# Kernel tuning notes

Hardware: AMD Instinct MI355X
Metric: run time of the kernel (lower is better)

## Reference

```python
import jax, jax.numpy as jnp
import numpy as np

B, T, F, H, E = 32, 512, 64, 64, 32  # batch, time, features(=sequence_length), hidden_dim, encoding_size


def setup_inputs() -> dict:
    key = jax.random.key(0)
    ks = jax.random.split(key, 14)
    sc = 0.05
    return {
        "x": jax.random.normal(ks[0], (B, T, F), jnp.float32),
        "s": jax.random.normal(ks[1], (B, T, E), jnp.float32),
        # gating FFN params
        "ffn_w1": jax.random.normal(ks[2], (F, H), jnp.float32) * sc,
        "ffn_b1": jnp.zeros((H,), jnp.float32),
        "ffn_w2": jax.random.normal(ks[3], (E, H), jnp.float32) * sc,
        "ffn_b2": jnp.zeros((H,), jnp.float32),
        "ffn_w3": jax.random.normal(ks[4], (H, F), jnp.float32) * sc,
        "ffn_b3": jnp.zeros((F,), jnp.float32),
        # per-feature expert FFN_j params (F experts, each Dense(1->H), ELU, Dense(H->H))
        "exp_w1": jax.random.normal(ks[5], (F, H), jnp.float32) * sc,  # weight of Dense(1->H) per feature
        "exp_b1": jnp.zeros((F, H), jnp.float32),
        "exp_w3": jax.random.normal(ks[6], (F, H, H), jnp.float32) * sc,
        "exp_b3": jnp.zeros((F, H), jnp.float32),
    }


def reference(x, s, ffn_w1, ffn_b1, ffn_w2, ffn_b2, ffn_w3, ffn_b3,
              exp_w1, exp_b1, exp_w3, exp_b3):
    # gating network: softmax over feature axis
    g = jnp.einsum('btf,fh->bth', x, ffn_w1) + ffn_b1 \
        + jnp.einsum('bte,eh->bth', s, ffn_w2) + ffn_b2
    logits = jnp.einsum('bth,hf->btf', jax.nn.elu(g), ffn_w3) + ffn_b3
    w_t = jax.nn.softmax(logits, axis=2)  # [B,T,F]

    # per-feature experts, batched: Dense(1->H) is a rank-1 outer product
    h = jax.nn.elu(x[..., None] * exp_w1[None, None] + exp_b1[None, None])  # [B,T,F,H]
    expert_out = jnp.einsum('btfh,fhk->btfk', h, exp_w3) + exp_b3[None, None]  # [B,T,F,H]

    # gate-weighted sum over features
    return jnp.einsum('btfk,btf->btk', expert_out, w_t)  # [B,T,H]
```

## Files before the change

### kernel.cpp

```cpp
#include <hip/hip_runtime.h>
#include <hip/hip_bf16.h>
#include <math.h>

#define NTOK 16384

typedef __attribute__((ext_vector_type(8))) short short8;
typedef __attribute__((ext_vector_type(4))) float f32x4;

__device__ __forceinline__ unsigned pack_bf16(float a, float b) {
    union { __hip_bfloat162 h; unsigned u; } cv;
    cv.h = __float22bfloat162_rn(make_float2(a, b));
    return cv.u;
}
__device__ __forceinline__ float eluf(float z) {
    return z > 0.0f ? z : (__expf(z) - 1.0f);
}

__global__ __launch_bounds__(256)
void prepass(const float* __restrict__ ew3, const float* __restrict__ eb3,
             unsigned short* __restrict__ ws) {
    __shared__ float tile[64 * 65];
    const int bid = blockIdx.x, tid = threadIdx.x;
    const float* src = (bid < 64) ? (ew3 + (size_t)bid * 4096) : eb3;

    const int r = tid >> 2, c0 = (tid & 3) * 16;
    #pragma unroll
    for (int j = 0; j < 4; ++j) {
        float4 v = *(const float4*)(src + r * 64 + c0 + j * 4);
        tile[r * 65 + c0 + j * 4 + 0] = v.x;
        tile[r * 65 + c0 + j * 4 + 1] = v.y;
        tile[r * 65 + c0 + j * 4 + 2] = v.z;
        tile[r * 65 + c0 + j * 4 + 3] = v.w;
    }
    __syncthreads();

    uint4* dst = (uint4*)(ws + (size_t)bid * 4096);
    #pragma unroll
    for (int it = 0; it < 2; ++it) {
        const int idx = tid + it * 256;
        const int c = idx >> 8, u = (idx >> 6) & 3, l = idx & 63;
        const int m = l & 15, q = (l >> 4) & 3;
        const int rb = c * 32 + q * 8, col = u * 16 + m;
        unsigned pw[4];
        #pragma unroll
        for (int p = 0; p < 4; ++p)
            pw[p] = pack_bf16(tile[(rb + 2 * p) * 65 + col],
                              tile[(rb + 2 * p + 1) * 65 + col]);
        uint4 pk; pk.x = pw[0]; pk.y = pw[1]; pk.z = pw[2]; pk.w = pw[3];
        dst[idx] = pk;
    }
}

__device__ __forceinline__ void gen_a2(const float* __restrict__ ew1,
                                       const float* __restrict__ eb1,
                                       int f, int quad,
                                       float xv0, float wt0, float xv1, float wt1,
                                       short8* a0, short8* a1) {
    #pragma unroll
    for (int c = 0; c < 2; ++c) {
        const float* w1p = ew1 + f * 64 + c * 32 + quad * 8;
        const float* b1p = eb1 + f * 64 + c * 32 + quad * 8;
        const float4 wa = *(const float4*)w1p, wb = *(const float4*)(w1p + 4);
        const float4 ba = *(const float4*)b1p, bb = *(const float4*)(b1p + 4);
        uint4 v0, v1;
        v0.x = pack_bf16(wt0 * eluf(fmaf(xv0, wa.x, ba.x)),
                         wt0 * eluf(fmaf(xv0, wa.y, ba.y)));
        v0.y = pack_bf16(wt0 * eluf(fmaf(xv0, wa.z, ba.z)),
                         wt0 * eluf(fmaf(xv0, wa.w, ba.w)));
        v0.z = pack_bf16(wt0 * eluf(fmaf(xv0, wb.x, bb.x)),
                         wt0 * eluf(fmaf(xv0, wb.y, bb.y)));
        v0.w = pack_bf16(wt0 * eluf(fmaf(xv0, wb.z, bb.z)),
                         wt0 * eluf(fmaf(xv0, wb.w, bb.w)));
        v1.x = pack_bf16(wt1 * eluf(fmaf(xv1, wa.x, ba.x)),
                         wt1 * eluf(fmaf(xv1, wa.y, ba.y)));
        v1.y = pack_bf16(wt1 * eluf(fmaf(xv1, wa.z, ba.z)),
                         wt1 * eluf(fmaf(xv1, wa.w, ba.w)));
        v1.z = pack_bf16(wt1 * eluf(fmaf(xv1, wb.x, bb.x)),
                         wt1 * eluf(fmaf(xv1, wb.y, bb.y)));
        v1.w = pack_bf16(wt1 * eluf(fmaf(xv1, wb.z, bb.z)),
                         wt1 * eluf(fmaf(xv1, wb.w, bb.w)));
        a0[c] = *(short8*)&v0;
        a1[c] = *(short8*)&v1;
    }
}

__global__ __launch_bounds__(512, 6)
void moe_main(const float* __restrict__ x,   const float* __restrict__ s,
              const float* __restrict__ fw1, const float* __restrict__ fb1,
              const float* __restrict__ fw2, const float* __restrict__ fb2,
              const float* __restrict__ fw3, const float* __restrict__ fb3,
              const float* __restrict__ ew1, const float* __restrict__ eb1,
              const float* __restrict__ ew3, const float* __restrict__ eb3,
              const unsigned short* __restrict__ img,
              float* __restrict__ out)
{
    __shared__ __align__(16) char smem[51840];
    float* xls = (float*)smem;
    float* wts = (float*)(smem + 8704);
    float* egs = (float*)(smem + 17024);
    float* ped0 = (float*)(smem + 17024);
    float* ped1 = (float*)(smem + 17024 + 17408);

    const int tid = threadIdx.x;
    const int wv = tid >> 6, lane = tid & 63;
    const int m = tid & 15, quad = (tid >> 4) & 3;
    const int tokbase = blockIdx.x * 32;

    {
        const int t = tid >> 4, fq = (tid & 15) * 4;
        *(float4*)&xls[t * 68 + fq] =
            *(const float4*)(x + (size_t)(tokbase + t) * 64 + fq);
    }
    __syncthreads();

    {
        const int t0w = wv * 4;
        const float* sw = s + (size_t)(tokbase + t0w) * 32;
        float g[4];
        const float b0 = fb1[lane] + fb2[lane];
        #pragma unroll
        for (int t = 0; t < 4; ++t) g[t] = b0;
        #pragma unroll 2
        for (int f = 0; f < 64; f += 4) {
            const float w0 = fw1[(f + 0) * 64 + lane];
            const float w1 = fw1[(f + 1) * 64 + lane];
            const float w2 = fw1[(f + 2) * 64 + lane];
            const float w3v = fw1[(f + 3) * 64 + lane];
            #pragma unroll
            for (int t = 0; t < 4; ++t) {
                const float4 xa = *(const float4*)&xls[(t0w + t) * 68 + f];
                g[t] = fmaf(xa.x, w0, fmaf(xa.y, w1, fmaf(xa.z, w2, fmaf(xa.w, w3v, g[t]))));
            }
        }
        #pragma unroll 2
        for (int e = 0; e < 32; e += 4) {
            const float w0 = fw2[(e + 0) * 64 + lane];
            const float w1 = fw2[(e + 1) * 64 + lane];
            const float w2 = fw2[(e + 2) * 64 + lane];
            const float w3v = fw2[(e + 3) * 64 + lane];
            #pragma unroll
            for (int t = 0; t < 4; ++t) {
                const float4 sa = *(const float4*)(sw + t * 32 + e);
                g[t] = fmaf(sa.x, w0, fmaf(sa.y, w1, fmaf(sa.z, w2, fmaf(sa.w, w3v, g[t]))));
            }
        }
        #pragma unroll
        for (int t = 0; t < 4; ++t) egs[(t0w + t) * 64 + lane] = eluf(g[t]);

        float lg[4];
        const float b3 = fb3[lane];
        #pragma unroll
        for (int t = 0; t < 4; ++t) lg[t] = b3;
        #pragma unroll 2
        for (int h = 0; h < 64; h += 4) {
            const float w0 = fw3[(h + 0) * 64 + lane];
            const float w1 = fw3[(h + 1) * 64 + lane];
            const float w2 = fw3[(h + 2) * 64 + lane];
            const float w3v = fw3[(h + 3) * 64 + lane];
            #pragma unroll
            for (int t = 0; t < 4; ++t) {
                const float4 ev = *(const float4*)&egs[(t0w + t) * 64 + h];
                lg[t] = fmaf(ev.x, w0, fmaf(ev.y, w1, fmaf(ev.z, w2, fmaf(ev.w, w3v, lg[t]))));
            }
        }
        #pragma unroll
        for (int t = 0; t < 4; ++t) {
            float mx = lg[t];
            #pragma unroll
            for (int off = 32; off > 0; off >>= 1) mx = fmaxf(mx, __shfl_xor(mx, off));
            const float p = __expf(lg[t] - mx);
            float sm = p;
            #pragma unroll
            for (int off = 32; off > 0; off >>= 1) sm += __shfl_xor(sm, off);
            wts[(t0w + t) * 65 + lane] = p / sm;
        }
    }
    __syncthreads();

    const int f0 = wv * 8;
    f32x4 acc0[4], acc1[4];
    #pragma unroll
    for (int u = 0; u < 4; ++u) {
        acc0[u] = (f32x4){0.f, 0.f, 0.f, 0.f};
        acc1[u] = (f32x4){0.f, 0.f, 0.f, 0.f};
    }

    const uint4* bp = (const uint4*)img + (size_t)f0 * 512 + lane;
    #pragma unroll 1
    for (int ff = 0; ff < 8; ++ff) {
        const int f = f0 + ff;
        uint4 b0 = bp[0 * 64];
        uint4 b1 = bp[1 * 64];
        uint4 b2 = bp[2 * 64];
        uint4 b3 = bp[3 * 64];
        uint4 b4 = bp[256 + 0 * 64];
        uint4 b5 = bp[256 + 1 * 64];
        uint4 b6 = bp[256 + 2 * 64];
        uint4 b7 = bp[256 + 3 * 64];
        bp += 512;
        const float xv0 = xls[m * 68 + f];
        const float wt0 = wts[m * 65 + f];
        const float xv1 = xls[(16 + m) * 68 + f];
        const float wt1 = wts[(16 + m) * 65 + f];
        short8 a0[2], a1[2];
        gen_a2(ew1, eb1, f, quad, xv0, wt0, xv1, wt1, a0, a1);
        acc0[0] = __builtin_amdgcn_mfma_f32_16x16x32_bf16(a0[0], *(short8*)&b0, acc0[0], 0, 0, 0);
        acc0[1] = __builtin_amdgcn_mfma_f32_16x16x32_bf16(a0[0], *(short8*)&b1, acc0[1], 0, 0, 0);
        acc0[2] = __builtin_amdgcn_mfma_f32_16x16x32_bf16(a0[0], *(short8*)&b2, acc0[2], 0, 0, 0);
        acc0[3] = __builtin_amdgcn_mfma_f32_16x16x32_bf16(a0[0], *(short8*)&b3, acc0[3], 0, 0, 0);
        acc1[0] = __builtin_amdgcn_mfma_f32_16x16x32_bf16(a1[0], *(short8*)&b0, acc1[0], 0, 0, 0);
        acc1[1] = __builtin_amdgcn_mfma_f32_16x16x32_bf16(a1[0], *(short8*)&b1, acc1[1], 0, 0, 0);
        acc1[2] = __builtin_amdgcn_mfma_f32_16x16x32_bf16(a1[0], *(short8*)&b2, acc1[2], 0, 0, 0);
        acc1[3] = __builtin_amdgcn_mfma_f32_16x16x32_bf16(a1[0], *(short8*)&b3, acc1[3], 0, 0, 0);
        acc0[0] = __builtin_amdgcn_mfma_f32_16x16x32_bf16(a0[1], *(short8*)&b4, acc0[0], 0, 0, 0);
        acc0[1] = __builtin_amdgcn_mfma_f32_16x16x32_bf16(a0[1], *(short8*)&b5, acc0[1], 0, 0, 0);
        acc0[2] = __builtin_amdgcn_mfma_f32_16x16x32_bf16(a0[1], *(short8*)&b6, acc0[2], 0, 0, 0);
        acc0[3] = __builtin_amdgcn_mfma_f32_16x16x32_bf16(a0[1], *(short8*)&b7, acc0[3], 0, 0, 0);
        acc1[0] = __builtin_amdgcn_mfma_f32_16x16x32_bf16(a1[1], *(short8*)&b4, acc1[0], 0, 0, 0);
        acc1[1] = __builtin_amdgcn_mfma_f32_16x16x32_bf16(a1[1], *(short8*)&b5, acc1[1], 0, 0, 0);
        acc1[2] = __builtin_amdgcn_mfma_f32_16x16x32_bf16(a1[1], *(short8*)&b6, acc1[2], 0, 0, 0);
        acc1[3] = __builtin_amdgcn_mfma_f32_16x16x32_bf16(a1[1], *(short8*)&b7, acc1[3], 0, 0, 0);
    }

    if (wv < 4) {
        const int tile = wv >> 1, eh = wv & 1;
        const int e0 = eh * 32 + quad * 8;
        const int trow = tile * 16 + m;
        uint4 av;
        av.x = pack_bf16(wts[trow * 65 + e0 + 0], wts[trow * 65 + e0 + 1]);
        av.y = pack_bf16(wts[trow * 65 + e0 + 2], wts[trow * 65 + e0 + 3]);
        av.z = pack_bf16(wts[trow * 65 + e0 + 4], wts[trow * 65 + e0 + 5]);
        av.w = pack_bf16(wts[trow * 65 + e0 + 6], wts[trow * 65 + e0 + 7]);
        short8 a = *(short8*)&av;
        const uint4* bq = (const uint4*)img + (size_t)64 * 512;
        f32x4* accT = tile ? acc1 : acc0;
        #pragma unroll
        for (int u = 0; u < 4; ++u) {
            uint4 bv = bq[eh * 256 + u * 64 + lane];
            accT[u] = __builtin_amdgcn_mfma_f32_16x16x32_bf16(a, *(short8*)&bv, accT[u], 0, 0, 0);
        }
    }

    if (wv >= 4) {
        #pragma unroll
        for (int u = 0; u < 4; ++u)
            #pragma unroll
            for (int r = 0; r < 4; ++r) {
                const int idx = (quad * 4 + r) * 68 + u * 16 + m;
                ped0[(wv - 4) * 1088 + idx] = acc0[u][r];
                ped1[(wv - 4) * 1088 + idx] = acc1[u][r];
            }
    }
    __syncthreads();
    if (wv < 4) {
        #pragma unroll
        for (int u = 0; u < 4; ++u)
            #pragma unroll
            for (int r = 0; r < 4; ++r) {
                const int idx = (quad * 4 + r) * 68 + u * 16 + m;
                acc0[u][r] += ped0[wv * 1088 + idx];
                acc1[u][r] += ped1[wv * 1088 + idx];
            }
    }
    __syncthreads();
    if (wv == 2 || wv == 3) {
        #pragma unroll
        for (int u = 0; u < 4; ++u)
            #pragma unroll
            for (int r = 0; r < 4; ++r) {
                const int idx = (quad * 4 + r) * 68 + u * 16 + m;
                ped0[(wv - 2) * 1088 + idx] = acc0[u][r];
                ped1[(wv - 2) * 1088 + idx] = acc1[u][r];
            }
    }
    __syncthreads();
    if (wv < 2) {
        #pragma unroll
        for (int u = 0; u < 4; ++u)
            #pragma unroll
            for (int r = 0; r < 4; ++r) {
                const int idx = (quad * 4 + r) * 68 + u * 16 + m;
                acc0[u][r] += ped0[wv * 1088 + idx];
                acc1[u][r] += ped1[wv * 1088 + idx];
            }
    }
    __syncthreads();
    if (wv == 1) {
        #pragma unroll
        for (int u = 0; u < 4; ++u)
            #pragma unroll
            for (int r = 0; r < 4; ++r) {
                const int idx = (quad * 4 + r) * 68 + u * 16 + m;
                ped0[idx] = acc0[u][r];
                ped1[idx] = acc1[u][r];
            }
    }
    __syncthreads();
    if (wv == 0) {
        #pragma unroll
        for (int u = 0; u < 4; ++u)
            #pragma unroll
            for (int r = 0; r < 4; ++r) {
                const int idx = (quad * 4 + r) * 68 + u * 16 + m;
                ped0[idx] += acc0[u][r];
                ped1[idx] += acc1[u][r];
            }
    }
    __syncthreads();

    {
        const int t = tid >> 4, kq = tid & 15;
        const float* srcp = (t < 16) ? &ped0[t * 68 + kq * 4]
                                     : &ped1[(t - 16) * 68 + kq * 4];
        *(float4*)(out + (size_t)(tokbase + t) * 64 + kq * 4) = *(const float4*)srcp;
    }
}

__device__ __forceinline__ void gen_a_fb(const float* __restrict__ ew1,
                                         const float* __restrict__ eb1,
                                         int f, int quad, float xv, float wt,
                                         short8* a) {
    #pragma unroll
    for (int c = 0; c < 2; ++c) {
        const float* w1p = ew1 + f * 64 + c * 32 + quad * 8;
        const float* b1p = eb1 + f * 64 + c * 32 + quad * 8;
        const float4 w1a = *(const float4*)w1p, w1b = *(const float4*)(w1p + 4);
        const float4 b1a = *(const float4*)b1p, b1b = *(const float4*)(b1p + 4);
        uint4 av;
        av.x = pack_bf16(wt * eluf(fmaf(xv, w1a.x, b1a.x)),
                         wt * eluf(fmaf(xv, w1a.y, b1a.y)));
        av.y = pack_bf16(wt * eluf(fmaf(xv, w1a.z, b1a.z)),
                         wt * eluf(fmaf(xv, w1a.w, b1a.w)));
        av.z = pack_bf16(wt * eluf(fmaf(xv, w1b.x, b1b.x)),
                         wt * eluf(fmaf(xv, w1b.y, b1b.y)));
        av.w = pack_bf16(wt * eluf(fmaf(xv, w1b.z, b1b.z)),
                         wt * eluf(fmaf(xv, w1b.w, b1b.w)));
        a[c] = *(short8*)&av;
    }
}
__device__ __forceinline__ void gen_b_fp32(const float* __restrict__ w3f,
                                           int quad, int m, short8 b[2][4]) {
    #pragma unroll
    for (int c = 0; c < 2; ++c)
        #pragma unroll
        for (int u = 0; u < 4; ++u) {
            const float* wp = w3f + (size_t)(c * 32 + quad * 8) * 64 + u * 16 + m;
            uint4 v;
            v.x = pack_bf16(wp[0],   wp[64]);
            v.y = pack_bf16(wp[128], wp[192]);
            v.z = pack_bf16(wp[256], wp[320]);
            v.w = pack_bf16(wp[384], wp[448]);
            b[c][u] = *(short8*)&v;
        }
}

__global__ __launch_bounds__(512, 8)
void moe_fb(const float* __restrict__ x,   const float* __restrict__ s,
            const float* __restrict__ fw1, const float* __restrict__ fb1,
            const float* __restrict__ fw2, const float* __restrict__ fb2,
            const float* __restrict__ fw3, const float* __restrict__ fb3,
            const float* __restrict__ ew1, const float* __restrict__ eb1,
            const float* __restrict__ ew3, const float* __restrict__ eb3,
            float* __restrict__ out)
{
    __shared__ __align__(16) float xls[16 * 68];
    __shared__ __align__(16) float wts[16 * 65];
    __shared__ __align__(16) float egs[16 * 64];
    __shared__ __align__(16) float ped[4][16 * 68];

    const int tid = threadIdx.x;
    const int wv = tid >> 6, lane = tid & 63;
    const int tokbase = blockIdx.x * 16;

    if (tid < 256) {
        const int t = tid >> 4, fq = (tid & 15) * 4;
        *(float4*)&xls[t * 68 + fq] =
            *(const float4*)(x + (size_t)(tokbase + t) * 64 + fq);
    }
    __syncthreads();
    {
        const int t0w = wv * 2;
        const float* sw = s + (size_t)(tokbase + t0w) * 32;
        float g0, g1;
        g0 = g1 = fb1[lane] + fb2[lane];
        #pragma unroll 2
        for (int ff = 0; ff < 64; ff += 4) {
            const float4 xa = *(const float4*)&xls[(t0w + 0) * 68 + ff];
            const float4 xb = *(const float4*)&xls[(t0w + 1) * 68 + ff];
            const float w0 = fw1[(ff + 0) * 64 + lane];
            const float w1 = fw1[(ff + 1) * 64 + lane];
            const float w2 = fw1[(ff + 2) * 64 + lane];
            const float w3v = fw1[(ff + 3) * 64 + lane];
            g0 = fmaf(xa.x, w0, fmaf(xa.y, w1, fmaf(xa.z, w2, fmaf(xa.w, w3v, g0))));
            g1 = fmaf(xb.x, w0, fmaf(xb.y, w1, fmaf(xb.z, w2, fmaf(xb.w, w3v, g1))));
        }
        #pragma unroll 2
        for (int e = 0; e < 32; e += 4) {
            const float4 sa = *(const float4*)(sw + e);
            const float4 sb = *(const float4*)(sw + 32 + e);
            const float w0 = fw2[(e + 0) * 64 + lane];
            const float w1 = fw2[(e + 1) * 64 + lane];
            const float w2 = fw2[(e + 2) * 64 + lane];
            const float w3v = fw2[(e + 3) * 64 + lane];
            g0 = fmaf(sa.x, w0, fmaf(sa.y, w1, fmaf(sa.z, w2, fmaf(sa.w, w3v, g0))));
            g1 = fmaf(sb.x, w0, fmaf(sb.y, w1, fmaf(sb.z, w2, fmaf(sb.w, w3v, g1))));
        }
        egs[(t0w + 0) * 64 + lane] = eluf(g0);
        egs[(t0w + 1) * 64 + lane] = eluf(g1);
        float lg0 = fb3[lane], lg1 = lg0;
        #pragma unroll 2
        for (int h = 0; h < 64; h += 4) {
            const float4 e0 = *(const float4*)&egs[(t0w + 0) * 64 + h];
            const float4 e1 = *(const float4*)&egs[(t0w + 1) * 64 + h];
            const float w0 = fw3[(h + 0) * 64 + lane];
            const float w1 = fw3[(h + 1) * 64 + lane];
            const float w2 = fw3[(h + 2) * 64 + lane];
            const float w3v = fw3[(h + 3) * 64 + lane];
            lg0 = fmaf(e0.x, w0, fmaf(e0.y, w1, fmaf(e0.z, w2, fmaf(e0.w, w3v, lg0))));
            lg1 = fmaf(e1.x, w0, fmaf(e1.y, w1, fmaf(e1.z, w2, fmaf(e1.w, w3v, lg1))));
        }
        float mx0 = lg0, mx1 = lg1;
        #pragma unroll
        for (int off = 32; off > 0; off >>= 1) {
            mx0 = fmaxf(mx0, __shfl_xor(mx0, off));
            mx1 = fmaxf(mx1, __shfl_xor(mx1, off));
        }
        const float p0 = __expf(lg0 - mx0), p1 = __expf(lg1 - mx1);
        float s0 = p0, s1 = p1;
        #pragma unroll
        for (int off = 32; off > 0; off >>= 1) {
            s0 += __shfl_xor(s0, off);
            s1 += __shfl_xor(s1, off);
        }
        wts[(t0w + 0) * 65 + lane] = p0 / s0;
        wts[(t0w + 1) * 65 + lane] = p1 / s1;
    }
    __syncthreads();

    const int m = tid & 15, quad = (tid >> 4) & 3;
    const int f0 = wv * 8;
    f32x4 acc[4];
    #pragma unroll
    for (int u = 0; u < 4; ++u) acc[u] = (f32x4){0.f, 0.f, 0.f, 0.f};

    #pragma unroll 1
    for (int ff = 0; ff < 8; ++ff) {
        const int fcur = f0 + ff;
        short8 b[2][4], a[2];
        gen_b_fp32(ew3 + (size_t)fcur * 4096, quad, m, b);
        gen_a_fb(ew1, eb1, fcur, quad, xls[m * 68 + fcur], wts[m * 65 + fcur], a);
        #pragma unroll
        for (int u = 0; u < 4; ++u) {
            acc[u] = __builtin_amdgcn_mfma_f32_16x16x32_bf16(a[0], b[0][u], acc[u], 0, 0, 0);
            acc[u] = __builtin_amdgcn_mfma_f32_16x16x32_bf16(a[1], b[1][u], acc[u], 0, 0, 0);
        }
    }
    if (wv < 2) {
        const int e0 = wv * 32 + quad * 8;
        uint4 av;
        av.x = pack_bf16(wts[m * 65 + e0 + 0], wts[m * 65 + e0 + 1]);
        av.y = pack_bf16(wts[m * 65 + e0 + 2], wts[m * 65 + e0 + 3]);
        av.z = pack_bf16(wts[m * 65 + e0 + 4], wts[m * 65 + e0 + 5]);
        av.w = pack_bf16(wts[m * 65 + e0 + 6], wts[m * 65 + e0 + 7]);
        short8 a = *(short8*)&av;
        #pragma unroll
        for (int u = 0; u < 4; ++u) {
            const float* wp = eb3 + (size_t)e0 * 64 + u * 16 + m;
            uint4 bv;
            bv.x = pack_bf16(wp[0],   wp[64]);
            bv.y = pack_bf16(wp[128], wp[192]);
            bv.z = pack_bf16(wp[256], wp[320]);
            bv.w = pack_bf16(wp[384], wp[448]);
            acc[u] = __builtin_amdgcn_mfma_f32_16x16x32_bf16(a, *(short8*)&bv, acc[u], 0, 0, 0);
        }
    }
    if (wv >= 4) {
        #pragma unroll
        for (int u = 0; u < 4; ++u)
            #pragma unroll
            for (int r = 0; r < 4; ++r)
                ped[wv - 4][(quad * 4 + r) * 68 + u * 16 + m] = acc[u][r];
    }
    __syncthreads();
    if (wv < 4) {
        #pragma unroll
        for (int u = 0; u < 4; ++u)
            #pragma unroll
            for (int r = 0; r < 4; ++r)
                acc[u][r] += ped[wv][(quad * 4 + r) * 68 + u * 16 + m];
    }
    __syncthreads();
    if (wv == 2 || wv == 3) {
        #pragma unroll
        for (int u = 0; u < 4; ++u)
            #pragma unroll
            for (int r = 0; r < 4; ++r)
                ped[wv - 2][(quad * 4 + r) * 68 + u * 16 + m] = acc[u][r];
    }
    __syncthreads();
    if (wv < 2) {
        #pragma unroll
        for (int u = 0; u < 4; ++u)
            #pragma unroll
            for (int r = 0; r < 4; ++r)
                acc[u][r] += ped[wv][(quad * 4 + r) * 68 + u * 16 + m];
    }
    __syncthreads();
    if (wv == 1) {
        #pragma unroll
        for (int u = 0; u < 4; ++u)
            #pragma unroll
            for (int r = 0; r < 4; ++r)
                ped[0][(quad * 4 + r) * 68 + u * 16 + m] = acc[u][r];
    }
    __syncthreads();
    if (wv == 0) {
        #pragma unroll
        for (int u = 0; u < 4; ++u)
            #pragma unroll
            for (int r = 0; r < 4; ++r)
                ped[0][(quad * 4 + r) * 68 + u * 16 + m] += acc[u][r];
    }
    __syncthreads();
    if (tid < 256) {
        const int t = tid >> 4, kq = tid & 15;
        float4 o = *(const float4*)&ped[0][t * 68 + kq * 4];
        *(float4*)(out + (size_t)(tokbase + t) * 64 + kq * 4) = o;
    }
}

extern "C" void kernel_launch(void* const* d_in, const int* in_sizes, int n_in,
                              void* d_out, int out_size, void* d_ws, size_t ws_size,
                              hipStream_t stream) {
    const float* x   = (const float*)d_in[0];
    const float* s   = (const float*)d_in[1];
    const float* fw1 = (const float*)d_in[2];
    const float* fb1 = (const float*)d_in[3];
    const float* fw2 = (const float*)d_in[4];
    const float* fb2 = (const float*)d_in[5];
    const float* fw3 = (const float*)d_in[6];
    const float* fb3 = (const float*)d_in[7];
    const float* ew1 = (const float*)d_in[8];
    const float* eb1 = (const float*)d_in[9];
    const float* ew3 = (const float*)d_in[10];
    const float* eb3 = (const float*)d_in[11];
    float* out = (float*)d_out;

    const size_t ws_need = (size_t)65 * 4096 * sizeof(unsigned short);
    if (ws_size >= ws_need && (((uintptr_t)d_ws & 15) == 0)) {
        unsigned short* img = (unsigned short*)d_ws;
        prepass<<<dim3(65), dim3(256), 0, stream>>>(ew3, eb3, img);
        moe_main<<<dim3(NTOK / 32), dim3(512), 0, stream>>>(
            x, s, fw1, fb1, fw2, fb2, fw3, fb3, ew1, eb1, ew3, eb3, img, out);
    } else {
        moe_fb<<<dim3(NTOK / 16), dim3(512), 0, stream>>>(
            x, s, fw1, fb1, fw2, fb2, fw3, fb3, ew1, eb1, ew3, eb3, out);
    }
}
```

Measured before the change: 123.7 us.

## Process 64 tokens per block and replace tree reduction with flat LDS sum

Each block now handles 64 tokens instead of 32, so every B fragment loaded from the bf16 weight image feeds four token tiles of MFMAs instead of two, halving weight traffic per token. The log-depth cross-wave reduction through shared memory becomes a per-tile staging step in which all 8 waves write partials and every thread sums 8 values. The cost is more accumulator registers (64 floats), larger LDS use, launch bounds lowered from 6 to 2 blocks per CU, and a grid of only 256 blocks, which may leave CUs underused.

```diff
diff --git a/kernel.cpp b/kernel.cpp
--- a/kernel.cpp
+++ b/kernel.cpp
@@ -51,40 +51,7 @@
     }
 }
 
-__device__ __forceinline__ void gen_a2(const float* __restrict__ ew1,
-                                       const float* __restrict__ eb1,
-                                       int f, int quad,
-                                       float xv0, float wt0, float xv1, float wt1,
-                                       short8* a0, short8* a1) {
-    #pragma unroll
-    for (int c = 0; c < 2; ++c) {
-        const float* w1p = ew1 + f * 64 + c * 32 + quad * 8;
-        const float* b1p = eb1 + f * 64 + c * 32 + quad * 8;
-        const float4 wa = *(const float4*)w1p, wb = *(const float4*)(w1p + 4);
-        const float4 ba = *(const float4*)b1p, bb = *(const float4*)(b1p + 4);
-        uint4 v0, v1;
-        v0.x = pack_bf16(wt0 * eluf(fmaf(xv0, wa.x, ba.x)),
-                         wt0 * eluf(fmaf(xv0, wa.y, ba.y)));
-        v0.y = pack_bf16(wt0 * eluf(fmaf(xv0, wa.z, ba.z)),
-                         wt0 * eluf(fmaf(xv0, wa.w, ba.w)));
-        v0.z = pack_bf16(wt0 * eluf(fmaf(xv0, wb.x, bb.x)),
-                         wt0 * eluf(fmaf(xv0, wb.y, bb.y)));
-        v0.w = pack_bf16(wt0 * eluf(fmaf(xv0, wb.z, bb.z)),
-                         wt0 * eluf(fmaf(xv0, wb.w, bb.w)));
-        v1.x = pack_bf16(wt1 * eluf(fmaf(xv1, wa.x, ba.x)),
-                         wt1 * eluf(fmaf(xv1, wa.y, ba.y)));
-        v1.y = pack_bf16(wt1 * eluf(fmaf(xv1, wa.z, ba.z)),
-                         wt1 * eluf(fmaf(xv1, wa.w, ba.w)));
-        v1.z = pack_bf16(wt1 * eluf(fmaf(xv1, wb.x, bb.x)),
-                         wt1 * eluf(fmaf(xv1, wb.y, bb.y)));
-        v1.w = pack_bf16(wt1 * eluf(fmaf(xv1, wb.z, bb.z)),
-                         wt1 * eluf(fmaf(xv1, wb.w, bb.w)));
-        a0[c] = *(short8*)&v0;
-        a1[c] = *(short8*)&v1;
-    }
-}
-
-__global__ __launch_bounds__(512, 6)
+__global__ __launch_bounds__(512, 2)
 void moe_main(const float* __restrict__ x,   const float* __restrict__ s,
               const float* __restrict__ fw1, const float* __restrict__ fb1,
               const float* __restrict__ fw2, const float* __restrict__ fb2,
@@ -94,32 +61,33 @@
               const unsigned short* __restrict__ img,
               float* __restrict__ out)
 {
-    __shared__ __align__(16) char smem[51840];
+    __shared__ __align__(16) char smem[68864];
     float* xls = (float*)smem;
-    float* wts = (float*)(smem + 8704);
-    float* egs = (float*)(smem + 17024);
-    float* ped0 = (float*)(smem + 17024);
-    float* ped1 = (float*)(smem + 17024 + 17408);
+    float* wts = (float*)(smem + 17408);
+    float* egs = (float*)(smem + 34048);
+    float* ped = (float*)(smem + 34048);
 
     const int tid = threadIdx.x;
     const int wv = tid >> 6, lane = tid & 63;
     const int m = tid & 15, quad = (tid >> 4) & 3;
-    const int tokbase = blockIdx.x * 32;
-
-    {
-        const int t = tid >> 4, fq = (tid & 15) * 4;
+    const int tokbase = blockIdx.x * 64;
+
+    #pragma unroll
+    for (int i = 0; i < 2; ++i) {
+        const int idx = tid + i * 512;
+        const int t = idx >> 4, fq = (idx & 15) * 4;
         *(float4*)&xls[t * 68 + fq] =
             *(const float4*)(x + (size_t)(tokbase + t) * 64 + fq);
     }
     __syncthreads();
 
     {
-        const int t0w = wv * 4;
+        const int t0w = wv * 8;
         const float* sw = s + (size_t)(tokbase + t0w) * 32;
-        float g[4];
+        float g[8];
         const float b0 = fb1[lane] + fb2[lane];
         #pragma unroll
-        for (int t = 0; t < 4; ++t) g[t] = b0;
+        for (int t = 0; t < 8; ++t) g[t] = b0;
         #pragma unroll 2
         for (int f = 0; f < 64; f += 4) {
             const float w0 = fw1[(f + 0) * 64 + lane];
@@ -127,7 +95,7 @@
             const float w2 = fw1[(f + 2) * 64 + lane];
             const float w3v = fw1[(f + 3) * 64 + lane];
             #pragma unroll
-            for (int t = 0; t < 4; ++t) {
+            for (int t = 0; t < 8; ++t) {
                 const float4 xa = *(const float4*)&xls[(t0w + t) * 68 + f];
                 g[t] = fmaf(xa.x, w0, fmaf(xa.y, w1, fmaf(xa.z, w2, fmaf(xa.w, w3v, g[t]))));
             }
@@ -139,18 +107,18 @@
             const float w2 = fw2[(e + 2) * 64 + lane];
             const float w3v = fw2[(e + 3) * 64 + lane];
             #pragma unroll
-            for (int t = 0; t < 4; ++t) {
+            for (int t = 0; t < 8; ++t) {
                 const float4 sa = *(const float4*)(sw + t * 32 + e);
                 g[t] = fmaf(sa.x, w0, fmaf(sa.y, w1, fmaf(sa.z, w2, fmaf(sa.w, w3v, g[t]))));
             }
         }
         #pragma unroll
-        for (int t = 0; t < 4; ++t) egs[(t0w + t) * 64 + lane] = eluf(g[t]);
-
-        float lg[4];
+        for (int t = 0; t < 8; ++t) egs[(t0w + t) * 64 + lane] = eluf(g[t]);
+
+        float lg[8];
         const float b3 = fb3[lane];
         #pragma unroll
-        for (int t = 0; t < 4; ++t) lg[t] = b3;
+        for (int t = 0; t < 8; ++t) lg[t] = b3;
         #pragma unroll 2
         for (int h = 0; h < 64; h += 4) {
             const float w0 = fw3[(h + 0) * 64 + lane];
@@ -158,13 +126,13 @@
             const float w2 = fw3[(h + 2) * 64 + lane];
             const float w3v = fw3[(h + 3) * 64 + lane];
             #pragma unroll
-            for (int t = 0; t < 4; ++t) {
+            for (int t = 0; t < 8; ++t) {
                 const float4 ev = *(const float4*)&egs[(t0w + t) * 64 + h];
                 lg[t] = fmaf(ev.x, w0, fmaf(ev.y, w1, fmaf(ev.z, w2, fmaf(ev.w, w3v, lg[t]))));
             }
         }
         #pragma unroll
-        for (int t = 0; t < 4; ++t) {
+        for (int t = 0; t < 8; ++t) {
             float mx = lg[t];
             #pragma unroll
             for (int off = 32; off > 0; off >>= 1) mx = fmaxf(mx, __shfl_xor(mx, off));
@@ -178,141 +146,95 @@
     __syncthreads();
 
     const int f0 = wv * 8;
-    f32x4 acc0[4], acc1[4];
-    #pragma unroll
-    for (int u = 0; u < 4; ++u) {
-        acc0[u] = (f32x4){0.f, 0.f, 0.f, 0.f};
-        acc1[u] = (f32x4){0.f, 0.f, 0.f, 0.f};
-    }
+    f32x4 acc[4][4];
+    #pragma unroll
+    for (int tl = 0; tl < 4; ++tl)
+        #pragma unroll
+        for (int u = 0; u < 4; ++u) acc[tl][u] = (f32x4){0.f, 0.f, 0.f, 0.f};
 
     const uint4* bp = (const uint4*)img + (size_t)f0 * 512 + lane;
-    #pragma unroll 1
+    #pragma unroll
     for (int ff = 0; ff < 8; ++ff) {
         const int f = f0 + ff;
-        uint4 b0 = bp[0 * 64];
-        uint4 b1 = bp[1 * 64];
-        uint4 b2 = bp[2 * 64];
-        uint4 b3 = bp[3 * 64];
-        uint4 b4 = bp[256 + 0 * 64];
-        uint4 b5 = bp[256 + 1 * 64];
-        uint4 b6 = bp[256 + 2 * 64];
-        uint4 b7 = bp[256 + 3 * 64];
+        uint4 B[8];
+        #pragma unroll
+        for (int i = 0; i < 8; ++i) B[i] = bp[(i >> 2) * 256 + (i & 3) * 64];
         bp += 512;
-        const float xv0 = xls[m * 68 + f];
-        const float wt0 = wts[m * 65 + f];
-        const float xv1 = xls[(16 + m) * 68 + f];
-        const float wt1 = wts[(16 + m) * 65 + f];
-        short8 a0[2], a1[2];
-        gen_a2(ew1, eb1, f, quad, xv0, wt0, xv1, wt1, a0, a1);
-        acc0[0] = __builtin_amdgcn_mfma_f32_16x16x32_bf16(a0[0], *(short8*)&b0, acc0[0], 0, 0, 0);
-        acc0[1] = __builtin_amdgcn_mfma_f32_16x16x32_bf16(a0[0], *(short8*)&b1, acc0[1], 0, 0, 0);
-        acc0[2] = __builtin_amdgcn_mfma_f32_16x16x32_bf16(a0[0], *(short8*)&b2, acc0[2], 0, 0, 0);
-        acc0[3] = __builtin_amdgcn_mfma_f32_16x16x32_bf16(a0[0], *(short8*)&b3, acc0[3], 0, 0, 0);
-        acc1[0] = __builtin_amdgcn_mfma_f32_16x16x32_bf16(a1[0], *(short8*)&b0, acc1[0], 0, 0, 0);
-        acc1[1] = __builtin_amdgcn_mfma_f32_16x16x32_bf16(a1[0], *(short8*)&b1, acc1[1], 0, 0, 0);
-        acc1[2] = __builtin_amdgcn_mfma_f32_16x16x32_bf16(a1[0], *(short8*)&b2, acc1[2], 0, 0, 0);
-        acc1[3] = __builtin_amdgcn_mfma_f32_16x16x32_bf16(a1[0], *(short8*)&b3, acc1[3], 0, 0, 0);
-        acc0[0] = __builtin_amdgcn_mfma_f32_16x16x32_bf16(a0[1], *(short8*)&b4, acc0[0], 0, 0, 0);
-        acc0[1] = __builtin_amdgcn_mfma_f32_16x16x32_bf16(a0[1], *(short8*)&b5, acc0[1], 0, 0, 0);
-        acc0[2] = __builtin_amdgcn_mfma_f32_16x16x32_bf16(a0[1], *(short8*)&b6, acc0[2], 0, 0, 0);
-        acc0[3] = __builtin_amdgcn_mfma_f32_16x16x32_bf16(a0[1], *(short8*)&b7, acc0[3], 0, 0, 0);
-        acc1[0] = __builtin_amdgcn_mfma_f32_16x16x32_bf16(a1[1], *(short8*)&b4, acc1[0], 0, 0, 0);
-        acc1[1] = __builtin_amdgcn_mfma_f32_16x16x32_bf16(a1[1], *(short8*)&b5, acc1[1], 0, 0, 0);
-        acc1[2] = __builtin_amdgcn_mfma_f32_16x16x32_bf16(a1[1], *(short8*)&b6, acc1[2], 0, 0, 0);
-        acc1[3] = __builtin_amdgcn_mfma_f32_16x16x32_bf16(a1[1], *(short8*)&b7, acc1[3], 0, 0, 0);
+        float xv[4], wt[4];
+        #pragma unroll
+        for (int tl = 0; tl < 4; ++tl) {
+            xv[tl] = xls[(tl * 16 + m) * 68 + f];
+            wt[tl] = wts[(tl * 16 + m) * 65 + f];
+        }
+        #pragma unroll
+        for (int c = 0; c < 2; ++c) {
+            const float* w1p = ew1 + f * 64 + c * 32 + quad * 8;
+            const float* b1p = eb1 + f * 64 + c * 32 + quad * 8;
+            const float4 wa = *(const float4*)w1p, wb = *(const float4*)(w1p + 4);
+            const float4 ba = *(const float4*)b1p, bb = *(const float4*)(b1p + 4);
+            const float wr[8] = {wa.x, wa.y, wa.z, wa.w, wb.x, wb.y, wb.z, wb.w};
+            const float br[8] = {ba.x, ba.y, ba.z, ba.w, bb.x, bb.y, bb.z, bb.w};
+            #pragma unroll
+            for (int tl = 0; tl < 4; ++tl) {
+                unsigned pw[4];
+                #pragma unroll
+                for (int p = 0; p < 4; ++p) {
+                    const float v0 = wt[tl] * eluf(fmaf(xv[tl], wr[2 * p],     br[2 * p]));
+                    const float v1 = wt[tl] * eluf(fmaf(xv[tl], wr[2 * p + 1], br[2 * p + 1]));
+                    pw[p] = pack_bf16(v0, v1);
+                }
+                uint4 av; av.x = pw[0]; av.y = pw[1]; av.z = pw[2]; av.w = pw[3];
+                const short8 a = *(short8*)&av;
+                acc[tl][0] = __builtin_amdgcn_mfma_f32_16x16x32_bf16(a, *(short8*)&B[c * 4 + 0], acc[tl][0], 0, 0, 0);
+                acc[tl][1] = __builtin_amdgcn_mfma_f32_16x16x32_bf16(a, *(short8*)&B[c * 4 + 1], acc[tl][1], 0, 0, 0);
+                acc[tl][2] = __builtin_amdgcn_mfma_f32_16x16x32_bf16(a, *(short8*)&B[c * 4 + 2], acc[tl][2], 0, 0, 0);
+                acc[tl][3] = __builtin_amdgcn_mfma_f32_16x16x32_bf16(a, *(short8*)&B[c * 4 + 3], acc[tl][3], 0, 0, 0);
+            }
+        }
     }
 
     if (wv < 4) {
-        const int tile = wv >> 1, eh = wv & 1;
-        const int e0 = eh * 32 + quad * 8;
-        const int trow = tile * 16 + m;
-        uint4 av;
-        av.x = pack_bf16(wts[trow * 65 + e0 + 0], wts[trow * 65 + e0 + 1]);
-        av.y = pack_bf16(wts[trow * 65 + e0 + 2], wts[trow * 65 + e0 + 3]);
-        av.z = pack_bf16(wts[trow * 65 + e0 + 4], wts[trow * 65 + e0 + 5]);
-        av.w = pack_bf16(wts[trow * 65 + e0 + 6], wts[trow * 65 + e0 + 7]);
-        short8 a = *(short8*)&av;
+        const int tl = wv;
+        const int trow = tl * 16 + m;
         const uint4* bq = (const uint4*)img + (size_t)64 * 512;
-        f32x4* accT = tile ? acc1 : acc0;
-        #pragma unroll
-        for (int u = 0; u < 4; ++u) {
-            uint4 bv = bq[eh * 256 + u * 64 + lane];
-            accT[u] = __builtin_amdgcn_mfma_f32_16x16x32_bf16(a, *(short8*)&bv, accT[u], 0, 0, 0);
-        }
-    }
-
-    if (wv >= 4) {
-        #pragma unroll
-        for (int u = 0; u < 4; ++u)
-            #pragma unroll
-            for (int r = 0; r < 4; ++r) {
-                const int idx = (quad * 4 + r) * 68 + u * 16 + m;
-                ped0[(wv - 4) * 1088 + idx] = acc0[u][r];
-                ped1[(wv - 4) * 1088 + idx] = acc1[u][r];
-            }
-    }
-    __syncthreads();
-    if (wv < 4) {
-        #pragma unroll
-        for (int u = 0; u < 4; ++u)
-            #pragma unroll
-            for (int r = 0; r < 4; ++r) {
-                const int idx = (quad * 4 + r) * 68 + u * 16 + m;
-                acc0[u][r] += ped0[wv * 1088 + idx];
-                acc1[u][r] += ped1[wv * 1088 + idx];
-            }
-    }
-    __syncthreads();
-    if (wv == 2 || wv == 3) {
-        #pragma unroll
-        for (int u = 0; u < 4; ++u)
-            #pragma unroll
-            for (int r = 0; r < 4; ++r) {
-                const int idx = (quad * 4 + r) * 68 + u * 16 + m;
-                ped0[(wv - 2) * 1088 + idx] = acc0[u][r];
-                ped1[(wv - 2) * 1088 + idx] = acc1[u][r];
-            }
-    }
-    __syncthreads();
-    if (wv < 2) {
-        #pragma unroll
-        for (int u = 0; u < 4; ++u)
-            #pragma unroll
-            for (int r = 0; r < 4; ++r) {
-                const int idx = (quad * 4 + r) * 68 + u * 16 + m;
-                acc0[u][r] += ped0[wv * 1088 + idx];
-                acc1[u][r] += ped1[wv * 1088 + idx];
-            }
-    }
-    __syncthreads();
-    if (wv == 1) {
-        #pragma unroll
-        for (int u = 0; u < 4; ++u)
-            #pragma unroll
-            for (int r = 0; r < 4; ++r) {
-                const int idx = (quad * 4 + r) * 68 + u * 16 + m;
-                ped0[idx] = acc0[u][r];
-                ped1[idx] = acc1[u][r];
-            }
-    }
-    __syncthreads();
-    if (wv == 0) {
-        #pragma unroll
-        for (int u = 0; u < 4; ++u)
-            #pragma unroll
-            for (int r = 0; r < 4; ++r) {
-                const int idx = (quad * 4 + r) * 68 + u * 16 + m;
-                ped0[idx] += acc0[u][r];
-                ped1[idx] += acc1[u][r];
-            }
-    }
-    __syncthreads();
-
-    {
-        const int t = tid >> 4, kq = tid & 15;
-        const float* srcp = (t < 16) ? &ped0[t * 68 + kq * 4]
-                                     : &ped1[(t - 16) * 68 + kq * 4];
-        *(float4*)(out + (size_t)(tokbase + t) * 64 + kq * 4) = *(const float4*)srcp;
+        #pragma unroll
+        for (int c = 0; c < 2; ++c) {
+            const int e0 = c * 32 + quad * 8;
+            uint4 av;
+            av.x = pack_bf16(wts[trow * 65 + e0 + 0], wts[trow * 65 + e0 + 1]);
+            av.y = pack_bf16(wts[trow * 65 + e0 + 2], wts[trow * 65 + e0 + 3]);
+            av.z = pack_bf16(wts[trow * 65 + e0 + 4], wts[trow * 65 + e0 + 5]);
+            av.w = pack_bf16(wts[trow * 65 + e0 + 6], wts[trow * 65 + e0 + 7]);
+            const short8 a = *(short8*)&av;
+            #pragma unroll
+            for (int u = 0; u < 4; ++u) {
+                uint4 bv = bq[c * 256 + u * 64 + lane];
+                acc[tl][u] = __builtin_amdgcn_mfma_f32_16x16x32_bf16(a, *(short8*)&bv, acc[tl][u], 0, 0, 0);
+            }
+        }
+    }
+
+    #pragma unroll 1
+    for (int tl = 0; tl < 4; ++tl) {
+        #pragma unroll
+        for (int u = 0; u < 4; ++u)
+            #pragma unroll
+            for (int r = 0; r < 4; ++r)
+                ped[wv * 1088 + (quad * 4 + r) * 68 + u * 16 + m] = acc[tl][u][r];
+        __syncthreads();
+        {
+            const int idx = tid * 2;
+            const int tr = idx >> 6, k = idx & 63;
+            float s0 = 0.f, s1 = 0.f;
+            #pragma unroll
+            for (int w = 0; w < 8; ++w) {
+                const float2 v = *(const float2*)&ped[w * 1088 + tr * 68 + k];
+                s0 += v.x; s1 += v.y;
+            }
+            *(float2*)(out + (size_t)(tokbase + tl * 16 + tr) * 64 + k) =
+                make_float2(s0, s1);
+        }
+        __syncthreads();
     }
 }
 
@@ -550,7 +472,7 @@
     if (ws_size >= ws_need && (((uintptr_t)d_ws & 15) == 0)) {
         unsigned short* img = (unsigned short*)d_ws;
         prepass<<<dim3(65), dim3(256), 0, stream>>>(ew3, eb3, img);
-        moe_main<<<dim3(NTOK / 32), dim3(512), 0, stream>>>(
+        moe_main<<<dim3(NTOK / 64), dim3(512), 0, stream>>>(
             x, s, fw1, fb1, fw2, fb2, fw3, fb3, ew1, eb1, ew3, eb3, img, out);
     } else {
         moe_fb<<<dim3(NTOK / 16), dim3(512), 0, stream>>>(
```

Result: slower. 240.6 us (+94.5%).
